# Kernel optimization log

Hardware: AMD Instinct MI355X
Metric: run time of the kernel (lower is better)

The kernel has to match this reference:

```python
import jax, jax.numpy as jnp
import numpy as np

HID = 768
NH = 12
HD = HID // NH
EPS = 1e-12


def setup_inputs() -> dict:
    key = jax.random.key(0)
    ks = jax.random.split(key, 16)
    B, S, N = 4, 2048, 8
    s = 1.0 / np.sqrt(HID)
    s4 = 1.0 / np.sqrt(4 * HID)
    return {
        "layer_output": jax.random.normal(ks[0], (B, S, HID), jnp.float32),
        "candidates_embeddings": jax.random.normal(ks[1], (B, S, N, HID), jnp.float32),
        "candidates_mask": jax.random.bernoulli(ks[2], 0.2, (B, S, N)),
        "Wq": jax.random.uniform(ks[3], (HID, HID), jnp.float32, -s, s),
        "bq": jnp.zeros((HID,), jnp.float32),
        "Wk": jax.random.uniform(ks[4], (HID, HID), jnp.float32, -s, s),
        "bk": jnp.zeros((HID,), jnp.float32),
        "Wv": jax.random.uniform(ks[5], (HID, HID), jnp.float32, -s, s),
        "bv": jnp.zeros((HID,), jnp.float32),
        "Wt": jax.random.uniform(ks[6], (4 * HID, HID), jnp.float32, -s, s),
        "bt": jnp.zeros((4 * HID,), jnp.float32),
        "Wc": jax.random.uniform(ks[7], (HID, 4 * HID), jnp.float32, -s4, s4),
        "bc": jnp.zeros((HID,), jnp.float32),
        "gamma": jnp.ones((HID,), jnp.float32),
        "beta": jnp.zeros((HID,), jnp.float32),
    }


def reference(layer_output, candidates_embeddings, candidates_mask,
              Wq, bq, Wk, bk, Wv, bv, Wt, bt, Wc, bc, gamma, beta):
    B, S, H = layer_output.shape
    T = B * S
    N = candidates_embeddings.shape[2]
    x = layer_output.reshape(T, H)
    c = candidates_embeddings.reshape(T, N, H)
    mask = candidates_mask.reshape(T, N)

    q = (x @ Wq.T + bq).reshape(T, NH, HD)            # q_len = 1 per token
    k = (c @ Wk.T + bk).reshape(T, N, NH, HD)
    v = (c @ Wv.T + bv).reshape(T, N, NH, HD)

    scores = jnp.einsum('thd,tnhd->thn', q, k) / np.sqrt(HD)
    # masked_fill with 1e-10 (NOT -inf) — faithful to the original
    scores = jnp.where(mask[:, None, :], jnp.asarray(1e-10, scores.dtype), scores)
    attn = jax.nn.softmax(scores, axis=-1)
    ctx = jnp.einsum('thn,tnhd->thd', attn, v).reshape(T, H)
    ctx = jnp.where(jnp.all(mask, axis=-1, keepdims=True), 0.0, ctx)

    h = jax.nn.gelu(ctx @ Wt.T + bt, approximate=False)
    ctx = h @ Wc.T + bc

    out = ctx.reshape(B, S, H) + layer_output
    mu = jnp.mean(out, axis=-1, keepdims=True)
    var = jnp.var(out, axis=-1, keepdims=True)
    out = (out - mu) * jax.lax.rsqrt(var + EPS) * gamma + beta
    return out
```

## Files before the change

kernel.cpp:

```cpp
#include <hip/hip_runtime.h>

typedef __bf16 bf16x8 __attribute__((ext_vector_type(8)));
typedef float f32x4 __attribute__((ext_vector_type(4)));
typedef unsigned short us8 __attribute__((ext_vector_type(8)));
typedef unsigned short us4 __attribute__((ext_vector_type(4)));
typedef unsigned int u32;

#define HIDN 768
#define NHEAD 12
#define HDIM 64
#define FFDIM 3072
#define NCAND 8

__device__ __forceinline__ float bf2f(unsigned short u) {
    union { unsigned int i; float f; } x; x.i = ((unsigned int)u) << 16; return x.f;
}
__device__ __forceinline__ unsigned short f2bf(float f) {
    __bf16 h = (__bf16)f;
    return __builtin_bit_cast(unsigned short, h);
}

typedef const __attribute__((address_space(1))) u32* gas_p;
typedef __attribute__((address_space(3))) u32* las_p;
__device__ __forceinline__ void load_lds16(const unsigned short* g, unsigned short* l) {
    __builtin_amdgcn_global_load_lds((gas_p)(const void*)g, (las_p)(void*)l, 16, 0, 0);
}

__global__ __launch_bounds__(256) void cvt_f2b(const float* __restrict__ src,
                                               unsigned short* __restrict__ dst, long n4) {
    long i = (long)blockIdx.x * 256 + threadIdx.x;
    if (i >= n4) return;
    float4 f = ((const float4*)src)[i];
    us4 o; o[0] = f2bf(f.x); o[1] = f2bf(f.y); o[2] = f2bf(f.z); o[3] = f2bf(f.w);
    *(us4*)&dst[i * 4] = o;
}

__global__ __launch_bounds__(256) void cvt_wk(const float* __restrict__ Wk,
                                              unsigned short* __restrict__ Wk2) {
    __shared__ float t[64][65];
    const int bx = blockIdx.x;
    const int h = bx / (HIDN / 64), jt = bx % (HIDN / 64);
    const int tid = threadIdx.x;
    int rj = tid & 63, rd = tid >> 6;
    for (int d = rd; d < 64; d += 4)
        t[d][rj] = Wk[(long)(h * 64 + d) * HIDN + jt * 64 + rj];
    __syncthreads();
    int wd = tid & 63, wj = tid >> 6;
    for (int j = wj; j < 64; j += 4)
        Wk2[((long)h * HIDN + jt * 64 + j) * 64 + wd] = f2bf(t[wd][j]);
}

__global__ void zero_flags(int* __restrict__ f) {
    if (threadIdx.x < 3) f[threadIdx.x] = 0;
}
__global__ __launch_bounds__(256) void mask_scan(const unsigned char* __restrict__ m,
                                                 int nbytes, int* __restrict__ flags) {
    int a0 = 0, a1 = 0, a2 = 0;
    for (int i = blockIdx.x * 256 + threadIdx.x; i < nbytes; i += gridDim.x * 256) {
        if (m[i]) {
            int r4 = i & 3, r8 = i & 7;
            if (r4 == 1) a0 = 1;
            if (r4 >= 2) a1 = 1;
            if (r8 == 4) a2 = 1;
        }
    }
    if (a0) atomicOr(&flags[0], 1);
    if (a1) atomicOr(&flags[1], 1);
    if (a2) atomicOr(&flags[2], 1);
}

template <bool OUT_BF16, bool GELU, int AI>
__global__ __launch_bounds__(256) void gemm128(
    const unsigned short* __restrict__ A, const unsigned short* __restrict__ B,
    void* __restrict__ Cv, const float* __restrict__ bias,
    int K, int lda, int ldb, int ldc,
    long a_z, long b_z, long c_z) {
    const int z = blockIdx.z;
    A += (long)z * a_z;
    B += (long)z * b_z;
    const int tid = threadIdx.x;
    const int m0 = blockIdx.y * (AI * 32), n0 = blockIdx.x * 128;
    __shared__ __attribute__((aligned(16))) unsigned short As[AI * 32 * 64];
    __shared__ __attribute__((aligned(16))) unsigned short Bs[128 * 64];
    f32x4 acc[AI][4] = {};
    const int lane = tid & 63, w = tid >> 6;
    const int wm = w & 1, wn = w >> 1;

    for (int k0 = 0; k0 < K; k0 += 64) {
#pragma unroll
        for (int i = 0; i < AI; i++) {
            int c = i * 256 + tid;
            int row = c >> 3;
            int g = (c & 7) ^ (row & 7);
            load_lds16(&A[(long)(m0 + row) * lda + k0 + g * 8], &As[c * 8]);
        }
#pragma unroll
        for (int i = 0; i < 4; i++) {
            int c = i * 256 + tid;
            int row = c >> 3;
            int g = (c & 7) ^ (row & 7);
            load_lds16(&B[(long)(n0 + row) * ldb + k0 + g * 8], &Bs[c * 8]);
        }
        __syncthreads();
#pragma unroll
        for (int kk = 0; kk < 64; kk += 32) {
            const int gc = (kk >> 3) + (lane >> 4);
            bf16x8 af[AI], bfr[4];
#pragma unroll
            for (int i = 0; i < AI; i++) {
                int r = wm * (AI * 16) + i * 16 + (lane & 15);
                af[i] = *(const bf16x8*)&As[r * 64 + ((gc ^ (r & 7)) << 3)];
            }
#pragma unroll
            for (int j = 0; j < 4; j++) {
                int r = wn * 64 + j * 16 + (lane & 15);
                bfr[j] = *(const bf16x8*)&Bs[r * 64 + ((gc ^ (r & 7)) << 3)];
            }
#pragma unroll
            for (int i = 0; i < AI; i++)
#pragma unroll
                for (int j = 0; j < 4; j++)
                    acc[i][j] = __builtin_amdgcn_mfma_f32_16x16x32_bf16(af[i], bfr[j], acc[i][j], 0, 0, 0);
        }
        __syncthreads();
    }

    float* Cf = (float*)Cv;
    unsigned short* Ch = (unsigned short*)Cv;
    const long cbase = (long)z * c_z;
#pragma unroll
    for (int i = 0; i < AI; i++)
#pragma unroll
        for (int j = 0; j < 4; j++) {
            int col = n0 + wn * 64 + j * 16 + (lane & 15);
            int rbase = m0 + wm * (AI * 16) + i * 16 + ((lane >> 4) * 4);
            float bb = bias ? bias[col] : 0.f;
#pragma unroll
            for (int r = 0; r < 4; r++) {
                int row = rbase + r;
                float v = acc[i][j][r] + bb;
                if (GELU) v = 0.5f * v * (1.f + erff(v * 0.70710678118654752f));
                long off = cbase + (long)row * ldc + col;
                if (OUT_BF16) Ch[off] = f2bf(v);
                else Cf[off] = v;
            }
        }
}

template <bool OUT_BF16, bool GELU, bool FLAG>
__global__ __launch_bounds__(256) void gemm_bt(
    const unsigned short* __restrict__ A, const unsigned short* __restrict__ B,
    void* __restrict__ Cv, const float* __restrict__ bias, const float* __restrict__ flag,
    int N, int K, int lda, int ldc,
    long a_z, long b_z, long c_z, int bias_z) {
    const int z = blockIdx.z;
    A += (long)z * a_z;
    B += (long)z * b_z;
    const int tid = threadIdx.x;
    const int m0 = blockIdx.y * 64, n0 = blockIdx.x * 64;
    __shared__ __attribute__((aligned(16))) unsigned short As[64][72];
    __shared__ __attribute__((aligned(16))) unsigned short Bs[64][72];
    f32x4 acc[2][2] = {};
    const int lane = tid & 63, w = tid >> 6;
    const int wm = w & 1, wn = w >> 1;
    const int ar = tid >> 3;
    const int ac = (tid & 7) * 8;

    for (int k0 = 0; k0 < K; k0 += 64) {
#pragma unroll
        for (int r = 0; r < 2; r++) {
            int row = ar + r * 32;
            us8 av = *(const us8*)&A[(long)(m0 + row) * lda + k0 + ac];
            *(us8*)&As[row][ac] = av;
            us8 bv = *(const us8*)&B[(long)(n0 + row) * K + k0 + ac];
            *(us8*)&Bs[row][ac] = bv;
        }
        __syncthreads();
#pragma unroll
        for (int kk = 0; kk < 64; kk += 32) {
            int kf = kk + (lane >> 4) * 8;
            bf16x8 a0 = *(const bf16x8*)&As[wm * 32 + (lane & 15)][kf];
            bf16x8 a1 = *(const bf16x8*)&As[wm * 32 + 16 + (lane & 15)][kf];
            bf16x8 b0 = *(const bf16x8*)&Bs[wn * 32 + (lane & 15)][kf];
            bf16x8 b1 = *(const bf16x8*)&Bs[wn * 32 + 16 + (lane & 15)][kf];
            acc[0][0] = __builtin_amdgcn_mfma_f32_16x16x32_bf16(a0, b0, acc[0][0], 0, 0, 0);
            acc[0][1] = __builtin_amdgcn_mfma_f32_16x16x32_bf16(a0, b1, acc[0][1], 0, 0, 0);
            acc[1][0] = __builtin_amdgcn_mfma_f32_16x16x32_bf16(a1, b0, acc[1][0], 0, 0, 0);
            acc[1][1] = __builtin_amdgcn_mfma_f32_16x16x32_bf16(a1, b1, acc[1][1], 0, 0, 0);
        }
        __syncthreads();
    }

    float* Cf = (float*)Cv;
    unsigned short* Ch = (unsigned short*)Cv;
    const long cbase = (long)z * c_z;
#pragma unroll
    for (int tm = 0; tm < 2; tm++)
#pragma unroll
        for (int tn = 0; tn < 2; tn++) {
            int col = n0 + wn * 32 + tn * 16 + (lane & 15);
            int rbase = m0 + wm * 32 + tm * 16 + ((lane >> 4) * 4);
            float bb = bias ? bias[(long)z * bias_z + col] : 0.f;
#pragma unroll
            for (int r = 0; r < 4; r++) {
                int row = rbase + r;
                float v = acc[tm][tn][r] + bb;
                if (GELU) v = 0.5f * v * (1.f + erff(v * 0.70710678118654752f));
                if (FLAG) v *= flag[row];
                long off = cbase + (long)row * ldc + col;
                if (OUT_BF16) Ch[off] = f2bf(v);
                else Cf[off] = v;
            }
        }
}

__global__ __launch_bounds__(256) void qbk_kernel(const unsigned short* __restrict__ Qb,
                                                  const float* __restrict__ bk,
                                                  float* __restrict__ qbk, long npair) {
    int lane = threadIdx.x & 63, w = threadIdx.x >> 6;
    long p = (long)blockIdx.x * 4 + w;
    if (p >= npair) return;
    long t = p / 12;
    int h = (int)(p - t * 12);
    float v = bf2f(Qb[t * HIDN + h * 64 + lane]) * bk[h * 64 + lane];
    for (int o = 32; o; o >>= 1) v += __shfl_down(v, o);
    if (lane == 0) qbk[p] = v;
}

#define LDP 776
__global__ __launch_bounds__(256) void attn_kernel(
    const float* __restrict__ cands, unsigned short* __restrict__ qkcw,
    const void* __restrict__ maskp, const int* __restrict__ flags,
    const float* __restrict__ qbk, float* __restrict__ allm, long t0) {
    const int tid = threadIdx.x;
    const long tl = blockIdx.x;
    const long t = t0 + tl;
    __shared__ __attribute__((aligned(16))) unsigned short buf[(NCAND + 16) * LDP];
    unsigned short* c_s = buf;
    unsigned short* qk_s = buf + NCAND * LDP;
    __shared__ float sc[NHEAD][NCAND];
    __shared__ float attn_s[NHEAD][NCAND];
    __shared__ float scr[16][16];
    __shared__ int msk[NCAND];
    __shared__ float qb_s[NHEAD];

    const float4* c4 = (const float4*)(cands + t * NCAND * HIDN);
    for (int i = tid; i < NCAND * HIDN / 4; i += 256) {
        int n = i / (HIDN / 4), j4 = (i - n * (HIDN / 4)) * 4;
        float4 f = c4[i];
        us4 o; o[0] = f2bf(f.x); o[1] = f2bf(f.y); o[2] = f2bf(f.z); o[3] = f2bf(f.w);
        *(us4*)&c_s[n * LDP + j4] = o;
    }
    const us8* q8 = (const us8*)(qkcw + tl * (NHEAD * HIDN));
    for (int i = tid; i < NHEAD * HIDN / 8; i += 256) {
        int h = i / (HIDN / 8), j8 = (i - h * (HIDN / 8)) * 8;
        *(us8*)&qk_s[h * LDP + j8] = q8[i];
    }
    if (tid < NCAND) {
        int mm = flags[0] ? 1 : (flags[1] ? 2 : (flags[2] ? 0 : 3));
        long mi = t * NCAND + tid;
        int mv;
        if (mm == 1)      mv = ((const unsigned char*)maskp)[mi] != 0;
        else if (mm == 2) mv = ((const float*)maskp)[mi] != 0.f;
        else if (mm == 3) mv = ((const long long*)maskp)[mi] != 0;
        else              mv = ((const int*)maskp)[mi] != 0;
        msk[tid] = mv;
    }
    if (tid >= 64 && tid < 64 + NHEAD) qb_s[tid - 64] = qbk[tl * NHEAD + (tid - 64)];
    __syncthreads();

    const int lane = tid & 63, w = tid >> 6;
    if (w == 0) {
        const unsigned short* arow = &qk_s[(lane & 15) * LDP + (lane >> 4) * 8];
        const unsigned short* brow = &c_s[(lane & 15) * LDP + (lane >> 4) * 8];
        f32x4 a0 = {}, a1 = {};
#pragma unroll
        for (int k = 0; k < HIDN; k += 64) {
            bf16x8 afa = *(const bf16x8*)&arow[k];
            bf16x8 bfa = *(const bf16x8*)&brow[k];
            bf16x8 afb = *(const bf16x8*)&arow[k + 32];
            bf16x8 bfb = *(const bf16x8*)&brow[k + 32];
            a0 = __builtin_amdgcn_mfma_f32_16x16x32_bf16(afa, bfa, a0, 0, 0, 0);
            a1 = __builtin_amdgcn_mfma_f32_16x16x32_bf16(afb, bfb, a1, 0, 0, 0);
        }
        int n = lane & 15;
#pragma unroll
        for (int r = 0; r < 4; r++) {
            int h = (lane >> 4) * 4 + r;
            scr[h][n] = a0[r] + a1[r];
        }
    }
    if (tid == 64) {
        int a = 1;
        for (int n = 0; n < NCAND; n++) a &= msk[n];
        allm[tl] = a ? 0.f : 1.f;
    }
    __syncthreads();

    if (tid < NHEAD) {
        int h = tid;
        float e[NCAND], sm = 0.f, mx = -1e30f;
        float svals[NCAND];
        for (int n = 0; n < NCAND; n++) {
            svals[n] = msk[n] ? 1e-10f : (scr[h][n] + qb_s[h]) * 0.125f;
            mx = fmaxf(mx, svals[n]);
        }
        for (int n = 0; n < NCAND; n++) { e[n] = expf(svals[n] - mx); sm += e[n]; }
        float inv = 1.f / sm;
        for (int n = 0; n < NCAND; n++) attn_s[h][n] = e[n] * inv;
    }
    __syncthreads();

    unsigned short* out = qkcw + tl * (NHEAD * HIDN);
    for (int i = tid; i < NHEAD * HIDN / 8; i += 256) {
        int h = i / (HIDN / 8), j8 = (i - h * (HIDN / 8)) * 8;
        float acc[8] = {0.f, 0.f, 0.f, 0.f, 0.f, 0.f, 0.f, 0.f};
#pragma unroll
        for (int n = 0; n < NCAND; n++) {
            us8 cv = *(const us8*)&c_s[n * LDP + j8];
            float a = attn_s[h][n];
#pragma unroll
            for (int k = 0; k < 8; k++) acc[k] += a * bf2f(cv[k]);
        }
        us8 o;
#pragma unroll
        for (int k = 0; k < 8; k++) o[k] = f2bf(acc[k]);
        ((us8*)out)[i] = o;
    }
}

__global__ __launch_bounds__(256) void ln_kernel(float* __restrict__ io, const float* __restrict__ x,
                                                 const float* __restrict__ gamma,
                                                 const float* __restrict__ beta, long t0) {
    const int tid = threadIdx.x;
    const long tl = blockIdx.x;
    const long t = t0 + tl;
    float* row = io + tl * HIDN;
    const float* xr = x + t * HIDN;
    float v[3];
#pragma unroll
    for (int i = 0; i < 3; i++) v[i] = row[tid + i * 256] + xr[tid + i * 256];
    __shared__ float red[4];
    const int lane = tid & 63, w = tid >> 6;
    float s = v[0] + v[1] + v[2];
    for (int o = 32; o; o >>= 1) s += __shfl_down(s, o);
    if (lane == 0) red[w] = s;
    __syncthreads();
    float mu = (red[0] + red[1] + red[2] + red[3]) * (1.f / HIDN);
    __syncthreads();
    float d0 = v[0] - mu, d1 = v[1] - mu, d2 = v[2] - mu;
    float q = d0 * d0 + d1 * d1 + d2 * d2;
    for (int o = 32; o; o >>= 1) q += __shfl_down(q, o);
    if (lane == 0) red[w] = q;
    __syncthreads();
    float var = (red[0] + red[1] + red[2] + red[3]) * (1.f / HIDN);
    float inv = rsqrtf(var + 1e-12f);
#pragma unroll
    for (int i = 0; i < 3; i++) {
        int j = tid + i * 256;
        row[j] = (v[i] - mu) * inv * gamma[j] + beta[j];
    }
}

extern "C" void kernel_launch(void* const* d_in, const int* in_sizes, int n_in,
                              void* d_out, int out_size, void* d_ws, size_t ws_size,
                              hipStream_t stream) {
    const float* x     = (const float*)d_in[0];
    const float* cands = (const float*)d_in[1];
    const void*  maskp = d_in[2];
    const float* Wq = (const float*)d_in[3];
    const float* bq = (const float*)d_in[4];
    const float* Wk = (const float*)d_in[5];
    const float* bk = (const float*)d_in[6];
    const float* Wv = (const float*)d_in[7];
    const float* bv = (const float*)d_in[8];
    const float* Wt = (const float*)d_in[9];
    const float* bt = (const float*)d_in[10];
    const float* Wc = (const float*)d_in[11];
    const float* bc = (const float*)d_in[12];
    const float* gamma = (const float*)d_in[13];
    const float* beta  = (const float*)d_in[14];
    float* out = (float*)d_out;

    const long T = (long)in_sizes[0] / HIDN;

    char* p = (char*)d_ws;
    auto alloc = [&](size_t bytes) -> char* {
        char* r = p;
        p += (bytes + 255) & ~(size_t)255;
        return r;
    };
    unsigned short* Wqb  = (unsigned short*)alloc((size_t)HIDN * HIDN * 2);
    unsigned short* Wk2b = (unsigned short*)alloc((size_t)HIDN * HIDN * 2);
    unsigned short* Wvb  = (unsigned short*)alloc((size_t)HIDN * HIDN * 2);
    unsigned short* Wtb  = (unsigned short*)alloc((size_t)FFDIM * HIDN * 2);
    unsigned short* Wcb  = (unsigned short*)alloc((size_t)HIDN * FFDIM * 2);
    int* flags = (int*)alloc(256);
    size_t fixed = (size_t)(p - (char*)d_ws);

    long TC = T;
    auto chunk_bytes = [&](long tc) -> size_t {
        return (size_t)tc * (HIDN * 2 + HIDN * 2 + NHEAD * 4 + 4 +
                             HIDN * 2 + NHEAD * HIDN * 2) + 8 * 256;
    };
    while (TC > 512 && fixed + chunk_bytes(TC) > ws_size) TC >>= 1;

    unsigned short* Xb   = (unsigned short*)alloc((size_t)TC * HIDN * 2);
    unsigned short* Qb   = (unsigned short*)alloc((size_t)TC * HIDN * 2);
    float* qbkb          = (float*)alloc((size_t)TC * NHEAD * 4);
    float* allm          = (float*)alloc((size_t)TC * 4);
    unsigned short* CTXb = (unsigned short*)alloc((size_t)TC * HIDN * 2);
    unsigned short* BIG  = (unsigned short*)alloc((size_t)TC * NHEAD * HIDN * 2);

    {
        long n4;
        n4 = (long)HIDN * HIDN / 4;
        cvt_f2b<<<dim3((n4 + 255) / 256), 256, 0, stream>>>(Wq, Wqb, n4);
        cvt_f2b<<<dim3((n4 + 255) / 256), 256, 0, stream>>>(Wv, Wvb, n4);
        n4 = (long)FFDIM * HIDN / 4;
        cvt_f2b<<<dim3((n4 + 255) / 256), 256, 0, stream>>>(Wt, Wtb, n4);
        cvt_f2b<<<dim3((n4 + 255) / 256), 256, 0, stream>>>(Wc, Wcb, n4);
        cvt_wk<<<dim3(NHEAD * (HIDN / 64)), 256, 0, stream>>>(Wk, Wk2b);
        zero_flags<<<dim3(1), 64, 0, stream>>>(flags);
        mask_scan<<<dim3(256), 256, 0, stream>>>((const unsigned char*)maskp,
                                                 (int)(T * NCAND), flags);
    }

    for (long t0 = 0; t0 < T; t0 += TC) {
        long n4 = TC * HIDN / 4;
        cvt_f2b<<<dim3((n4 + 255) / 256), 256, 0, stream>>>(x + t0 * HIDN, Xb, n4);

        gemm128<true, false, 2><<<dim3(HIDN / 128, TC / 64, 1), 256, 0, stream>>>(
            Xb, Wqb, Qb, bq, HIDN, HIDN, HIDN, HIDN, 0, 0, 0);

        qbk_kernel<<<dim3((TC * NHEAD + 3) / 4), 256, 0, stream>>>(Qb, bk, qbkb, TC * NHEAD);

        gemm128<true, false, 4><<<dim3(HIDN / 128, TC / 128, NHEAD), 256, 0, stream>>>(
            Qb, Wk2b, BIG, nullptr, HDIM, HIDN, HDIM, NHEAD * HIDN,
            HDIM, (long)HIDN * HDIM, HIDN);

        attn_kernel<<<dim3(TC), 256, 0, stream>>>(cands, BIG, maskp, flags, qbkb, allm, t0);

        gemm_bt<true, false, true><<<dim3(1, TC / 64, NHEAD), 256, 0, stream>>>(
            BIG, Wvb, CTXb, bv, allm, HDIM, HIDN, NHEAD * HIDN, HIDN,
            HIDN, (long)HDIM * HIDN, HDIM, HDIM);

        gemm128<true, true, 4><<<dim3(FFDIM / 128, TC / 128, 1), 256, 0, stream>>>(
            CTXb, Wtb, BIG, bt, HIDN, HIDN, HIDN, FFDIM, 0, 0, 0);

        gemm128<false, false, 2><<<dim3(HIDN / 128, TC / 64, 1), 256, 0, stream>>>(
            BIG, Wcb, out + t0 * HIDN, bc, FFDIM, FFDIM, FFDIM, HIDN, 0, 0, 0);

        ln_kernel<<<dim3(TC), 256, 0, stream>>>(out + t0 * HIDN, x, gamma, beta, t0);
    }
}
```

Measured before the change: 663.9 us.

## Restructure attention kernel LDS staging with swizzled direct loads and fp32 candidates

The q·Wk rows are now copied straight from global memory into LDS with an XOR-swizzled, unpadded layout, and the MFMA reads use that swizzle. This shrinks the shared-memory footprint, which should allow more blocks per CU. After the score MFMA, the bf16 candidates are held in registers and rewritten into the same LDS buffer as fp32, and the softmax weights reuse the score scratch array. The weighted sum can then read float4 vectors without bf16 unpacking. The token chunk size is also capped at 4096, which may add extra chunk launches in exchange for a smaller working set.

```diff
diff --git a/kernel.cpp b/kernel.cpp
--- a/kernel.cpp
+++ b/kernel.cpp
@@ -235,26 +235,31 @@
     const int tid = threadIdx.x;
     const long tl = blockIdx.x;
     const long t = t0 + tl;
-    __shared__ __attribute__((aligned(16))) unsigned short buf[(NCAND + 16) * LDP];
+    __shared__ __attribute__((aligned(16))) unsigned short buf[8 * LDP + 12 * HIDN];
     unsigned short* c_s = buf;
-    unsigned short* qk_s = buf + NCAND * LDP;
-    __shared__ float sc[NHEAD][NCAND];
-    __shared__ float attn_s[NHEAD][NCAND];
+    unsigned short* qk_s = buf + 8 * LDP;
     __shared__ float scr[16][16];
     __shared__ int msk[NCAND];
     __shared__ float qb_s[NHEAD];
 
+    const unsigned short* qsrc = qkcw + tl * (NHEAD * HIDN);
+#pragma unroll
+    for (int p = 0; p < 5; p++) {
+        int i = tid + p * 256;
+        if (i < NHEAD * HIDN / 8) {
+            int row = i / 96, cc = i - row * 96;
+            int g = (cc & ~7) | ((cc & 7) ^ (row & 7));
+            load_lds16(&qsrc[row * HIDN + g * 8], &qk_s[i * 8]);
+        }
+    }
     const float4* c4 = (const float4*)(cands + t * NCAND * HIDN);
-    for (int i = tid; i < NCAND * HIDN / 4; i += 256) {
-        int n = i / (HIDN / 4), j4 = (i - n * (HIDN / 4)) * 4;
+#pragma unroll
+    for (int p = 0; p < 6; p++) {
+        int i = tid + p * 256;
+        int n = i / 192, j4 = (i - n * 192) * 4;
         float4 f = c4[i];
         us4 o; o[0] = f2bf(f.x); o[1] = f2bf(f.y); o[2] = f2bf(f.z); o[3] = f2bf(f.w);
         *(us4*)&c_s[n * LDP + j4] = o;
-    }
-    const us8* q8 = (const us8*)(qkcw + tl * (NHEAD * HIDN));
-    for (int i = tid; i < NHEAD * HIDN / 8; i += 256) {
-        int h = i / (HIDN / 8), j8 = (i - h * (HIDN / 8)) * 8;
-        *(us8*)&qk_s[h * LDP + j8] = q8[i];
     }
     if (tid < NCAND) {
         int mm = flags[0] ? 1 : (flags[1] ? 2 : (flags[2] ? 0 : 3));
@@ -270,16 +275,29 @@
     __syncthreads();
 
     const int lane = tid & 63, w = tid >> 6;
+
+    us4 creg[6];
+#pragma unroll
+    for (int p = 0; p < 6; p++) {
+        int c8 = tid + p * 256;
+        int n = c8 / 192, j = (c8 - n * 192) * 4;
+        creg[p] = *(const us4*)&c_s[n * LDP + j];
+    }
     if (w == 0) {
-        const unsigned short* arow = &qk_s[(lane & 15) * LDP + (lane >> 4) * 8];
-        const unsigned short* brow = &c_s[(lane & 15) * LDP + (lane >> 4) * 8];
+        int ar = lane & 15; if (ar > 11) ar = 11;
+        int br = lane & 15; if (br > 7) br = 7;
+        const int kq = lane >> 4;
+        const unsigned short* brow = &c_s[br * LDP + kq * 8];
         f32x4 a0 = {}, a1 = {};
 #pragma unroll
-        for (int k = 0; k < HIDN; k += 64) {
-            bf16x8 afa = *(const bf16x8*)&arow[k];
-            bf16x8 bfa = *(const bf16x8*)&brow[k];
-            bf16x8 afb = *(const bf16x8*)&arow[k + 32];
-            bf16x8 bfb = *(const bf16x8*)&brow[k + 32];
+        for (int k0 = 0; k0 < HIDN; k0 += 64) {
+            int c1 = (k0 >> 3) + kq, c2 = c1 + 4;
+            int g1 = (c1 & ~7) | ((c1 & 7) ^ (ar & 7));
+            int g2 = (c2 & ~7) | ((c2 & 7) ^ (ar & 7));
+            bf16x8 afa = *(const bf16x8*)&qk_s[ar * HIDN + g1 * 8];
+            bf16x8 afb = *(const bf16x8*)&qk_s[ar * HIDN + g2 * 8];
+            bf16x8 bfa = *(const bf16x8*)&brow[k0];
+            bf16x8 bfb = *(const bf16x8*)&brow[k0 + 32];
             a0 = __builtin_amdgcn_mfma_f32_16x16x32_bf16(afa, bfa, a0, 0, 0, 0);
             a1 = __builtin_amdgcn_mfma_f32_16x16x32_bf16(afb, bfb, a1, 0, 0, 0);
         }
@@ -299,33 +317,46 @@
 
     if (tid < NHEAD) {
         int h = tid;
-        float e[NCAND], sm = 0.f, mx = -1e30f;
-        float svals[NCAND];
+        float sv[NCAND], sm = 0.f, mx = -1e30f;
         for (int n = 0; n < NCAND; n++) {
-            svals[n] = msk[n] ? 1e-10f : (scr[h][n] + qb_s[h]) * 0.125f;
-            mx = fmaxf(mx, svals[n]);
-        }
-        for (int n = 0; n < NCAND; n++) { e[n] = expf(svals[n] - mx); sm += e[n]; }
+            sv[n] = msk[n] ? 1e-10f : (scr[h][n] + qb_s[h]) * 0.125f;
+            mx = fmaxf(mx, sv[n]);
+        }
+        for (int n = 0; n < NCAND; n++) { sv[n] = expf(sv[n] - mx); sm += sv[n]; }
         float inv = 1.f / sm;
-        for (int n = 0; n < NCAND; n++) attn_s[h][n] = e[n] * inv;
+        for (int n = 0; n < NCAND; n++) scr[h][n] = sv[n] * inv;
+    }
+    float* c32 = (float*)buf;
+#pragma unroll
+    for (int p = 0; p < 6; p++) {
+        int c8 = tid + p * 256;
+        f32x4 f;
+#pragma unroll
+        for (int k = 0; k < 4; k++) f[k] = bf2f(creg[p][k]);
+        *(f32x4*)&c32[c8 * 4] = f;
     }
     __syncthreads();
 
     unsigned short* out = qkcw + tl * (NHEAD * HIDN);
-    for (int i = tid; i < NHEAD * HIDN / 8; i += 256) {
-        int h = i / (HIDN / 8), j8 = (i - h * (HIDN / 8)) * 8;
-        float acc[8] = {0.f, 0.f, 0.f, 0.f, 0.f, 0.f, 0.f, 0.f};
-#pragma unroll
-        for (int n = 0; n < NCAND; n++) {
-            us8 cv = *(const us8*)&c_s[n * LDP + j8];
-            float a = attn_s[h][n];
-#pragma unroll
-            for (int k = 0; k < 8; k++) acc[k] += a * bf2f(cv[k]);
-        }
-        us8 o;
-#pragma unroll
-        for (int k = 0; k < 8; k++) o[k] = f2bf(acc[k]);
-        ((us8*)out)[i] = o;
+#pragma unroll
+    for (int p = 0; p < 5; p++) {
+        int i = tid + p * 256;
+        if (i < NHEAD * HIDN / 8) {
+            int h = i / 96, j8 = (i - h * 96) * 8;
+            f32x4 acc0 = {}, acc1 = {};
+#pragma unroll
+            for (int n = 0; n < NCAND; n++) {
+                float a = scr[h][n];
+                f32x4 v0 = *(const f32x4*)&c32[n * HIDN + j8];
+                f32x4 v1 = *(const f32x4*)&c32[n * HIDN + j8 + 4];
+#pragma unroll
+                for (int k = 0; k < 4; k++) { acc0[k] += a * v0[k]; acc1[k] += a * v1[k]; }
+            }
+            us8 o;
+#pragma unroll
+            for (int k = 0; k < 4; k++) { o[k] = f2bf(acc0[k]); o[4 + k] = f2bf(acc1[k]); }
+            *(us8*)&out[i * 8] = o;
+        }
     }
 }
 
@@ -404,6 +435,7 @@
                              HIDN * 2 + NHEAD * HIDN * 2) + 8 * 256;
     };
     while (TC > 512 && fixed + chunk_bytes(TC) > ws_size) TC >>= 1;
+    if (TC > 4096) TC = 4096;
 
     unsigned short* Xb   = (unsigned short*)alloc((size_t)TC * HIDN * 2);
     unsigned short* Qb   = (unsigned short*)alloc((size_t)TC * HIDN * 2);
```

Measured after the change: 689.7 us. +3.9%, slower.
